# Performance work log

Hardware: AMD Instinct MI355X
Metric: run time of the kernel (lower is better)

Reference implementation:

```python
import jax, jax.numpy as jnp
import numpy as np

N_NODES = 50000


def gcn_conv(x, src, dst, W, b, num_nodes):
    """PyG GCNConv: y = D^{-1/2} (A + I) D^{-1/2} (x @ W) + b.
    src/dst already include self-loops."""
    h = x @ W  # [N, F_out]
    deg = jax.ops.segment_sum(jnp.ones_like(dst, dtype=h.dtype), dst,
                              num_segments=num_nodes)  # in-degree incl. self-loop
    dinv = jnp.where(deg > 0, jax.lax.rsqrt(deg), 0.0)
    norm = dinv[src] * dinv[dst]  # [E]
    msgs = h[src] * norm[:, None]  # gather + scale, [E, F_out]
    out = jax.ops.segment_sum(msgs, dst, num_segments=num_nodes)
    return out + b


def setup_inputs() -> dict:
    key = jax.random.key(0)
    k1, k2, k3, k4 = jax.random.split(key, 4)
    latent, hidden, out_ch = 64, 128, 64
    n_edges = 800000
    z = jax.random.normal(k1, (N_NODES, latent), dtype=jnp.float32)
    edge_index = jax.random.randint(k2, (2, n_edges), 0, N_NODES, dtype=jnp.int64)
    # Glorot-style scaled weights
    W1 = jax.random.normal(k3, (latent, hidden), dtype=jnp.float32) * (1.0 / np.sqrt(latent))
    b1 = jnp.zeros((hidden,), dtype=jnp.float32)
    W2 = jax.random.normal(k4, (hidden, out_ch), dtype=jnp.float32) * (1.0 / np.sqrt(hidden))
    b2 = jnp.zeros((out_ch,), dtype=jnp.float32)
    return {"z": z, "edge_index": edge_index, "W1": W1, "b1": b1, "W2": W2, "b2": b2}


def reference(z, edge_index, W1, b1, W2, b2):
    num_nodes = z.shape[0]
    loops = jnp.arange(num_nodes, dtype=edge_index.dtype)
    src = jnp.concatenate([edge_index[0], loops])  # add self-loops
    dst = jnp.concatenate([edge_index[1], loops])
    x = gcn_conv(z, src, dst, W1, b1, num_nodes)
    x = jax.nn.relu(x)
    x = gcn_conv(x, src, dst, W2, b2, num_nodes)
    x = jax.nn.relu(x)
    return x
```

## Files before the change

### kernel.cpp

```cpp
#include <hip/hip_runtime.h>
#include <hip/hip_fp16.h>

static inline size_t align256(size_t x){ return (x + 255) & ~(size_t)255; }

#define CAP 64
#define NPART 8

__device__ __forceinline__ int detect_is64(const unsigned* __restrict__ e){
  unsigned v = e[2 * (threadIdx.x & 63) + 1];
  return (__ballot(v != 0u) == 0ull) ? 1 : 0;
}

__device__ __forceinline__ int load_idx(const void* edges, long i, int is64){
  return is64 ? (int)((const long long*)edges)[i] : ((const int*)edges)[i];
}

__global__ __launch_bounds__(256) void pack_kernel(const void* __restrict__ edges, int E,
                                                   unsigned* __restrict__ pe,
                                                   int* __restrict__ cnt, int N){
  const int is64 = detect_is64((const unsigned*)edges);
  const int t0 = blockIdx.x * 256 + threadIdx.x;
  const int stride = gridDim.x * 256;
  for (int i = t0; i < N; i += stride) cnt[i] = 0;
  for (int i = t0; i < E; i += stride){
    const unsigned s = (unsigned)load_idx(edges, i, is64);
    const unsigned d = (unsigned)load_idx(edges, (long)E + i, is64);
    pe[i] = (d << 16) | (s & 0xFFFFu);
  }
}

__global__ __launch_bounds__(256) void build_kernel(const unsigned* __restrict__ pe, int E,
                                                    int* __restrict__ cnt,
                                                    unsigned short* __restrict__ csr,
                                                    int N){
  const int p  = blockIdx.x & (NPART - 1);
  const int q  = blockIdx.x >> 3;
  const int nq = gridDim.x >> 3;
  const int nper = (N + NPART - 1) / NPART;
  const int lo = p * nper;
  const int hi = min(lo + nper, N);
  const int stride = nq * 256;
  for (int i = q * 256 + threadIdx.x; i < E; i += stride){
    const unsigned v = pe[i];
    const int d = (int)(v >> 16);
    if (d < lo || d >= hi) continue;
    const int pos = atomicAdd(&cnt[d], 1);
    if (pos < CAP) csr[((size_t)d << 6) + pos] = (unsigned short)(v & 0xFFFFu);
  }
}

__device__ __forceinline__ void h8_acc(uint4 r, float* a){
  const __half2* h = (const __half2*)&r;
  #pragma unroll
  for (int k = 0; k < 4; ++k){
    const float2 f = __half22float2(h[k]);
    a[2*k]     += f.x;
    a[2*k + 1] += f.y;
  }
}

__device__ __forceinline__ void gather8(const uint4* __restrict__ H,
                                        const unsigned short* __restrict__ row,
                                        int deg, int j, float* a){
  int e = 0;
  #pragma unroll 1
  for (; e + 4 <= deg; e += 4){
    const ushort4 rr = *(const ushort4*)(row + e);
    const uint4 v0 = H[(size_t)rr.x * 8 + j];
    const uint4 v1 = H[(size_t)rr.y * 8 + j];
    const uint4 v2 = H[(size_t)rr.z * 8 + j];
    const uint4 v3 = H[(size_t)rr.w * 8 + j];
    h8_acc(v0, a); h8_acc(v1, a); h8_acc(v2, a); h8_acc(v3, a);
  }
  #pragma unroll 1
  for (; e < deg; ++e) h8_acc(H[(size_t)row[e] * 8 + j], a);
}

__global__ __launch_bounds__(256) void prep_kernel(const float4* __restrict__ z,
                                                   uint4* __restrict__ zh,
                                                   const int* __restrict__ cnt,
                                                   float* __restrict__ dinv, int N){
  const int idx = blockIdx.x * 256 + threadIdx.x;
  const int node = idx >> 3;
  if (node >= N) return;
  const int j = idx & 7;
  const float di = rsqrtf((float)(cnt[node] + 1));
  if (j == 0) dinv[node] = di;
  const float4 v0 = z[(size_t)node * 16 + j * 2];
  const float4 v1 = z[(size_t)node * 16 + j * 2 + 1];
  const __half2 a0 = __float22half2_rn(make_float2(di * v0.x, di * v0.y));
  const __half2 a1 = __float22half2_rn(make_float2(di * v0.z, di * v0.w));
  const __half2 a2 = __float22half2_rn(make_float2(di * v1.x, di * v1.y));
  const __half2 a3 = __float22half2_rn(make_float2(di * v1.z, di * v1.w));
  uint4 r;
  r.x = *(const unsigned*)&a0; r.y = *(const unsigned*)&a1;
  r.z = *(const unsigned*)&a2; r.w = *(const unsigned*)&a3;
  zh[idx] = r;
}

__global__ __launch_bounds__(512) void agg_gemm1_kernel(const uint4* __restrict__ zh,
                                                        const unsigned short* __restrict__ csr,
                                                        const int* __restrict__ cnt,
                                                        const float* __restrict__ dinv,
                                                        const float* __restrict__ W1,
                                                        const float* __restrict__ b1,
                                                        float* __restrict__ x1, int N){
  __shared__ float Wl[64 * 128];
  __shared__ float rows[64 * 64];
  const int t = threadIdx.x;

  {
    const float4* Wg = (const float4*)W1;
    float4* Wd = (float4*)Wl;
    #pragma unroll
    for (int i = 0; i < 4; ++i) Wd[t + i * 512] = Wg[t + i * 512];
  }

  const int local = t >> 3;
  const int j = t & 7;
  const int node = blockIdx.x * 64 + local;
  float a[8] = {0.f, 0.f, 0.f, 0.f, 0.f, 0.f, 0.f, 0.f};
  if (node < N){
    h8_acc(zh[(size_t)node * 8 + j], a);
    const int deg = min(cnt[node], CAP);
    gather8(zh, csr + ((size_t)node << 6), deg, j, a);
    const float di = dinv[node];
    #pragma unroll
    for (int k = 0; k < 8; ++k) a[k] *= di;
  }
  float4* rp = (float4*)&rows[t * 8];
  rp[0] = make_float4(a[0], a[1], a[2], a[3]);
  rp[1] = make_float4(a[4], a[5], a[6], a[7]);
  __syncthreads();

  const int jc = t & 127;
  const int g = t >> 7;
  const float bv = b1[jc];
  float accv[16];
  #pragma unroll
  for (int n = 0; n < 16; ++n) accv[n] = bv;

  #pragma unroll 2
  for (int k4 = 0; k4 < 16; ++k4){
    const float w0 = Wl[(4 * k4 + 0) * 128 + jc];
    const float w1 = Wl[(4 * k4 + 1) * 128 + jc];
    const float w2 = Wl[(4 * k4 + 2) * 128 + jc];
    const float w3 = Wl[(4 * k4 + 3) * 128 + jc];
    #pragma unroll
    for (int n = 0; n < 16; ++n){
      const float4 r = ((const float4*)rows)[(g * 16 + n) * 16 + k4];
      accv[n] = fmaf(r.x, w0, accv[n]);
      accv[n] = fmaf(r.y, w1, accv[n]);
      accv[n] = fmaf(r.z, w2, accv[n]);
      accv[n] = fmaf(r.w, w3, accv[n]);
    }
  }

  #pragma unroll
  for (int n = 0; n < 16; ++n){
    const int nn = blockIdx.x * 64 + g * 16 + n;
    if (nn < N) x1[(size_t)nn * 128 + jc] = fmaxf(accv[n], 0.0f);
  }
}

__global__ __launch_bounds__(256) void agg2_kernel(const uint4* __restrict__ X,
                                                   float4* __restrict__ Y,
                                                   const unsigned short* __restrict__ csr,
                                                   const int* __restrict__ cnt,
                                                   const float* __restrict__ dinv,
                                                   const float4* __restrict__ bias,
                                                   int N){
  const int local = threadIdx.x >> 3;
  const int j = threadIdx.x & 7;
  const int node = blockIdx.x * 32 + local;
  if (node >= N) return;
  float a[8] = {0.f, 0.f, 0.f, 0.f, 0.f, 0.f, 0.f, 0.f};
  h8_acc(X[(size_t)node * 8 + j], a);
  const int deg = min(cnt[node], CAP);
  gather8(X, csr + ((size_t)node << 6), deg, j, a);
  const float di = dinv[node];
  const float4 b0 = bias[j * 2];
  const float4 b1v = bias[j * 2 + 1];
  float4 o0, o1;
  o0.x = fmaxf(fmaf(di, a[0], b0.x), 0.f);
  o0.y = fmaxf(fmaf(di, a[1], b0.y), 0.f);
  o0.z = fmaxf(fmaf(di, a[2], b0.z), 0.f);
  o0.w = fmaxf(fmaf(di, a[3], b0.w), 0.f);
  o1.x = fmaxf(fmaf(di, a[4], b1v.x), 0.f);
  o1.y = fmaxf(fmaf(di, a[5], b1v.y), 0.f);
  o1.z = fmaxf(fmaf(di, a[6], b1v.z), 0.f);
  o1.w = fmaxf(fmaf(di, a[7], b1v.w), 0.f);
  Y[(size_t)node * 16 + j * 2] = o0;
  Y[(size_t)node * 16 + j * 2 + 1] = o1;
}

__global__ __launch_bounds__(256) void gemm2_kernel(const float* __restrict__ X,
                                                    const float* __restrict__ W,
                                                    const float* __restrict__ dinv,
                                                    __half* __restrict__ Y, int N){
  constexpr int FIN = 128, FOUT = 64, NT = 32;
  constexpr int G = 256 / FOUT;
  constexpr int NTG = NT / G;
  __shared__ float Wl[FIN * FOUT];
  __shared__ float rows[NT * FIN];
  const int t = threadIdx.x;
  const int node0 = blockIdx.x * NT;

  {
    const float4* Wg = (const float4*)W;
    float4* Wd = (float4*)Wl;
    #pragma unroll
    for (int i = 0; i < FIN * FOUT / 4 / 256; ++i) Wd[t + i * 256] = Wg[t + i * 256];
  }
  {
    float4* rd = (float4*)rows;
    const float4* Xg = (const float4*)X;
    constexpr int TOT = NT * FIN / 4;
    #pragma unroll
    for (int i = 0; i < TOT / 256; ++i){
      const int id = t + i * 256;
      const int n = id / (FIN / 4);
      const int k4 = id % (FIN / 4);
      int node = node0 + n; if (node > N - 1) node = N - 1;
      rd[id] = Xg[(size_t)node * (FIN / 4) + k4];
    }
  }
  __syncthreads();

  const int j = t % FOUT;
  const int g = t / FOUT;
  float acc[NTG];
  #pragma unroll
  for (int n = 0; n < NTG; ++n) acc[n] = 0.0f;

  #pragma unroll 2
  for (int k4 = 0; k4 < FIN / 4; ++k4){
    const float w0 = Wl[(4 * k4 + 0) * FOUT + j];
    const float w1 = Wl[(4 * k4 + 1) * FOUT + j];
    const float w2 = Wl[(4 * k4 + 2) * FOUT + j];
    const float w3 = Wl[(4 * k4 + 3) * FOUT + j];
    #pragma unroll
    for (int n = 0; n < NTG; ++n){
      const float4 r = ((const float4*)rows)[(g * NTG + n) * (FIN / 4) + k4];
      acc[n] = fmaf(r.x, w0, acc[n]);
      acc[n] = fmaf(r.y, w1, acc[n]);
      acc[n] = fmaf(r.z, w2, acc[n]);
      acc[n] = fmaf(r.w, w3, acc[n]);
    }
  }

  #pragma unroll
  for (int n = 0; n < NTG; ++n){
    const int node = node0 + g * NTG + n;
    if (node < N) Y[(size_t)node * FOUT + j] = __float2half(acc[n] * dinv[node]);
  }
}

extern "C" void kernel_launch(void* const* d_in, const int* in_sizes, int n_in,
                              void* d_out, int out_size, void* d_ws, size_t ws_size,
                              hipStream_t stream){
  const float* z  = (const float*)d_in[0];
  const void*  edges = d_in[1];
  const float* W1 = (const float*)d_in[2];
  const float* b1 = (const float*)d_in[3];
  const float* W2 = (const float*)d_in[4];
  const float* b2 = (const float*)d_in[5];
  float* out = (float*)d_out;

  constexpr int F0 = 64, F1 = 128;
  const int N = in_sizes[0] / F0;
  const int E = in_sizes[1] / 2;
  (void)n_in; (void)out_size;

  char* p = (char*)d_ws;
  int*            cnt  = (int*)p;            p += align256((size_t)N * 4);
  float*          dinv = (float*)p;          p += align256((size_t)N * 4);
  unsigned short* csr  = (unsigned short*)p; p += align256((size_t)N * CAP * 2);
  unsigned*       pe   = (unsigned*)p;       p += align256((size_t)E * 4);
  __half*         hbuf = (__half*)p;         p += align256((size_t)N * F0 * 2);
  float*          x1   = (float*)p;          p += align256((size_t)N * F1 * 4);
  (void)ws_size;
  __half* zh = hbuf;
  __half* h2 = hbuf;

  pack_kernel<<<1024, 256, 0, stream>>>(edges, E, pe, cnt, N);
  build_kernel<<<1024, 256, 0, stream>>>(pe, E, cnt, csr, N);
  prep_kernel<<<(N * 8 + 255) / 256, 256, 0, stream>>>(
      (const float4*)z, (uint4*)zh, cnt, dinv, N);

  agg_gemm1_kernel<<<(N + 63) / 64, 512, 0, stream>>>(
      (const uint4*)zh, csr, cnt, dinv, W1, b1, x1, N);

  gemm2_kernel<<<(N + 31) / 32, 256, 0, stream>>>(x1, W2, dinv, h2, N);
  agg2_kernel<<<(N + 31) / 32, 256, 0, stream>>>(
      (const uint4*)h2, (float4*)out, csr, cnt, dinv, (const float4*)b2, N);
}
```

Measured before the change: 199.8 us.

## Fuse second-layer GEMM into first aggregation kernel via shared-memory fp16 tile

Merges gemm2 into the agg+gemm1 kernel. The relu'd hidden activations stay in shared memory as fp16 and are multiplied by W2 right away, so the fp32 x1 buffer of N*128 floats is never written to or read from global memory, and one launch disappears. W1 and W2 are staged in shared memory as fp16 to fit the extra tile, which lowers the precision of the weights and hidden activations. The larger shared-memory footprint and the extra barriers may reduce occupancy of the fused kernel.

```diff
diff --git a/kernel.cpp b/kernel.cpp
--- a/kernel.cpp
+++ b/kernel.cpp
@@ -98,22 +98,31 @@
   zh[idx] = r;
 }
 
-__global__ __launch_bounds__(512) void agg_gemm1_kernel(const uint4* __restrict__ zh,
-                                                        const unsigned short* __restrict__ csr,
-                                                        const int* __restrict__ cnt,
-                                                        const float* __restrict__ dinv,
-                                                        const float* __restrict__ W1,
-                                                        const float* __restrict__ b1,
-                                                        float* __restrict__ x1, int N){
-  __shared__ float Wl[64 * 128];
+#define X1LD 132
+__global__ __launch_bounds__(512) void fused1_kernel(const uint4* __restrict__ zh,
+                                                     const unsigned short* __restrict__ csr,
+                                                     const int* __restrict__ cnt,
+                                                     const float* __restrict__ dinv,
+                                                     const float* __restrict__ W1,
+                                                     const float* __restrict__ b1,
+                                                     const float* __restrict__ W2,
+                                                     __half* __restrict__ h2, int N){
+  __shared__ unsigned short wl[64 * 128];
   __shared__ float rows[64 * 64];
+  __shared__ unsigned short x1t[64 * X1LD];
   const int t = threadIdx.x;
 
   {
     const float4* Wg = (const float4*)W1;
-    float4* Wd = (float4*)Wl;
-    #pragma unroll
-    for (int i = 0; i < 4; ++i) Wd[t + i * 512] = Wg[t + i * 512];
+    #pragma unroll
+    for (int c = 0; c < 4; ++c){
+      const int gi = t + c * 512;
+      const float4 v = Wg[gi];
+      const __half2 h0 = __float22half2_rn(make_float2(v.x, v.y));
+      const __half2 h1 = __float22half2_rn(make_float2(v.z, v.w));
+      uint2 r; r.x = *(const unsigned*)&h0; r.y = *(const unsigned*)&h1;
+      *(uint2*)&wl[gi * 4] = r;
+    }
   }
 
   const int local = t >> 3;
@@ -135,31 +144,97 @@
 
   const int jc = t & 127;
   const int g = t >> 7;
-  const float bv = b1[jc];
-  float accv[16];
-  #pragma unroll
-  for (int n = 0; n < 16; ++n) accv[n] = bv;
-
-  #pragma unroll 2
-  for (int k4 = 0; k4 < 16; ++k4){
-    const float w0 = Wl[(4 * k4 + 0) * 128 + jc];
-    const float w1 = Wl[(4 * k4 + 1) * 128 + jc];
-    const float w2 = Wl[(4 * k4 + 2) * 128 + jc];
-    const float w3 = Wl[(4 * k4 + 3) * 128 + jc];
+  {
+    const float bv = b1[jc];
+    float accv[16];
+    #pragma unroll
+    for (int n = 0; n < 16; ++n) accv[n] = bv;
+
+    #pragma unroll 2
+    for (int k4 = 0; k4 < 16; ++k4){
+      const float w0 = __half2float(*(const __half*)&wl[(4 * k4 + 0) * 128 + jc]);
+      const float w1 = __half2float(*(const __half*)&wl[(4 * k4 + 1) * 128 + jc]);
+      const float w2 = __half2float(*(const __half*)&wl[(4 * k4 + 2) * 128 + jc]);
+      const float w3 = __half2float(*(const __half*)&wl[(4 * k4 + 3) * 128 + jc]);
+      #pragma unroll
+      for (int n = 0; n < 16; ++n){
+        const float4 r = ((const float4*)rows)[(g * 16 + n) * 16 + k4];
+        accv[n] = fmaf(r.x, w0, accv[n]);
+        accv[n] = fmaf(r.y, w1, accv[n]);
+        accv[n] = fmaf(r.z, w2, accv[n]);
+        accv[n] = fmaf(r.w, w3, accv[n]);
+      }
+    }
     #pragma unroll
     for (int n = 0; n < 16; ++n){
-      const float4 r = ((const float4*)rows)[(g * 16 + n) * 16 + k4];
-      accv[n] = fmaf(r.x, w0, accv[n]);
-      accv[n] = fmaf(r.y, w1, accv[n]);
-      accv[n] = fmaf(r.z, w2, accv[n]);
-      accv[n] = fmaf(r.w, w3, accv[n]);
-    }
-  }
-
-  #pragma unroll
-  for (int n = 0; n < 16; ++n){
-    const int nn = blockIdx.x * 64 + g * 16 + n;
-    if (nn < N) x1[(size_t)nn * 128 + jc] = fmaxf(accv[n], 0.0f);
+      const __half hv = __float2half(fmaxf(accv[n], 0.0f));
+      x1t[(g * 16 + n) * X1LD + jc] = *(const unsigned short*)&hv;
+    }
+  }
+  __syncthreads();
+
+  {
+    const float4* Wg = (const float4*)W2;
+    #pragma unroll
+    for (int c = 0; c < 4; ++c){
+      const int gi = t + c * 512;
+      const float4 v = Wg[gi];
+      const __half2 h0 = __float22half2_rn(make_float2(v.x, v.y));
+      const __half2 h1 = __float22half2_rn(make_float2(v.z, v.w));
+      uint2 r; r.x = *(const unsigned*)&h0; r.y = *(const unsigned*)&h1;
+      *(uint2*)&wl[gi * 4] = r;
+    }
+  }
+  __syncthreads();
+
+  const int cg = t & 15;
+  const int ng = t >> 4;
+  const int n0 = ng * 2, n1 = n0 + 1;
+  float acc0[4] = {0.f,0.f,0.f,0.f}, acc1[4] = {0.f,0.f,0.f,0.f};
+  #pragma unroll 4
+  for (int k4 = 0; k4 < 32; ++k4){
+    const int k = k4 * 4;
+    const uint2 xa = *(const uint2*)&x1t[n0 * X1LD + k];
+    const uint2 xb = *(const uint2*)&x1t[n1 * X1LD + k];
+    float xf0[4], xf1[4];
+    {
+      const float2 p0 = __half22float2(*(const __half2*)&xa.x);
+      const float2 p1 = __half22float2(*(const __half2*)&xa.y);
+      xf0[0]=p0.x; xf0[1]=p0.y; xf0[2]=p1.x; xf0[3]=p1.y;
+      const float2 q0 = __half22float2(*(const __half2*)&xb.x);
+      const float2 q1 = __half22float2(*(const __half2*)&xb.y);
+      xf1[0]=q0.x; xf1[1]=q0.y; xf1[2]=q1.x; xf1[3]=q1.y;
+    }
+    #pragma unroll
+    for (int dk = 0; dk < 4; ++dk){
+      const uint2 wv = *(const uint2*)&wl[(k + dk) * 64 + cg * 4];
+      const float2 w01 = __half22float2(*(const __half2*)&wv.x);
+      const float2 w23 = __half22float2(*(const __half2*)&wv.y);
+      acc0[0] = fmaf(xf0[dk], w01.x, acc0[0]);
+      acc0[1] = fmaf(xf0[dk], w01.y, acc0[1]);
+      acc0[2] = fmaf(xf0[dk], w23.x, acc0[2]);
+      acc0[3] = fmaf(xf0[dk], w23.y, acc0[3]);
+      acc1[0] = fmaf(xf1[dk], w01.x, acc1[0]);
+      acc1[1] = fmaf(xf1[dk], w01.y, acc1[1]);
+      acc1[2] = fmaf(xf1[dk], w23.x, acc1[2]);
+      acc1[3] = fmaf(xf1[dk], w23.y, acc1[3]);
+    }
+  }
+  const int gn0 = blockIdx.x * 64 + n0;
+  const int gn1 = gn0 + 1;
+  if (gn0 < N){
+    const float d0 = dinv[gn0];
+    const __half2 h0 = __float22half2_rn(make_float2(acc0[0]*d0, acc0[1]*d0));
+    const __half2 h1 = __float22half2_rn(make_float2(acc0[2]*d0, acc0[3]*d0));
+    uint2 r; r.x = *(const unsigned*)&h0; r.y = *(const unsigned*)&h1;
+    *(uint2*)&h2[(size_t)gn0 * 64 + cg * 4] = r;
+  }
+  if (gn1 < N){
+    const float d1 = dinv[gn1];
+    const __half2 h0 = __float22half2_rn(make_float2(acc1[0]*d1, acc1[1]*d1));
+    const __half2 h1 = __float22half2_rn(make_float2(acc1[2]*d1, acc1[3]*d1));
+    uint2 r; r.x = *(const unsigned*)&h0; r.y = *(const unsigned*)&h1;
+    *(uint2*)&h2[(size_t)gn1 * 64 + cg * 4] = r;
   }
 }
 
@@ -194,68 +269,6 @@
   Y[(size_t)node * 16 + j * 2 + 1] = o1;
 }
 
-__global__ __launch_bounds__(256) void gemm2_kernel(const float* __restrict__ X,
-                                                    const float* __restrict__ W,
-                                                    const float* __restrict__ dinv,
-                                                    __half* __restrict__ Y, int N){
-  constexpr int FIN = 128, FOUT = 64, NT = 32;
-  constexpr int G = 256 / FOUT;
-  constexpr int NTG = NT / G;
-  __shared__ float Wl[FIN * FOUT];
-  __shared__ float rows[NT * FIN];
-  const int t = threadIdx.x;
-  const int node0 = blockIdx.x * NT;
-
-  {
-    const float4* Wg = (const float4*)W;
-    float4* Wd = (float4*)Wl;
-    #pragma unroll
-    for (int i = 0; i < FIN * FOUT / 4 / 256; ++i) Wd[t + i * 256] = Wg[t + i * 256];
-  }
-  {
-    float4* rd = (float4*)rows;
-    const float4* Xg = (const float4*)X;
-    constexpr int TOT = NT * FIN / 4;
-    #pragma unroll
-    for (int i = 0; i < TOT / 256; ++i){
-      const int id = t + i * 256;
-      const int n = id / (FIN / 4);
-      const int k4 = id % (FIN / 4);
-      int node = node0 + n; if (node > N - 1) node = N - 1;
-      rd[id] = Xg[(size_t)node * (FIN / 4) + k4];
-    }
-  }
-  __syncthreads();
-
-  const int j = t % FOUT;
-  const int g = t / FOUT;
-  float acc[NTG];
-  #pragma unroll
-  for (int n = 0; n < NTG; ++n) acc[n] = 0.0f;
-
-  #pragma unroll 2
-  for (int k4 = 0; k4 < FIN / 4; ++k4){
-    const float w0 = Wl[(4 * k4 + 0) * FOUT + j];
-    const float w1 = Wl[(4 * k4 + 1) * FOUT + j];
-    const float w2 = Wl[(4 * k4 + 2) * FOUT + j];
-    const float w3 = Wl[(4 * k4 + 3) * FOUT + j];
-    #pragma unroll
-    for (int n = 0; n < NTG; ++n){
-      const float4 r = ((const float4*)rows)[(g * NTG + n) * (FIN / 4) + k4];
-      acc[n] = fmaf(r.x, w0, acc[n]);
-      acc[n] = fmaf(r.y, w1, acc[n]);
-      acc[n] = fmaf(r.z, w2, acc[n]);
-      acc[n] = fmaf(r.w, w3, acc[n]);
-    }
-  }
-
-  #pragma unroll
-  for (int n = 0; n < NTG; ++n){
-    const int node = node0 + g * NTG + n;
-    if (node < N) Y[(size_t)node * FOUT + j] = __float2half(acc[n] * dinv[node]);
-  }
-}
-
 extern "C" void kernel_launch(void* const* d_in, const int* in_sizes, int n_in,
                               void* d_out, int out_size, void* d_ws, size_t ws_size,
                               hipStream_t stream){
@@ -267,7 +280,7 @@
   const float* b2 = (const float*)d_in[5];
   float* out = (float*)d_out;
 
-  constexpr int F0 = 64, F1 = 128;
+  constexpr int F0 = 64;
   const int N = in_sizes[0] / F0;
   const int E = in_sizes[1] / 2;
   (void)n_in; (void)out_size;
@@ -277,21 +290,18 @@
   float*          dinv = (float*)p;          p += align256((size_t)N * 4);
   unsigned short* csr  = (unsigned short*)p; p += align256((size_t)N * CAP * 2);
   unsigned*       pe   = (unsigned*)p;       p += align256((size_t)E * 4);
-  __half*         hbuf = (__half*)p;         p += align256((size_t)N * F0 * 2);
-  float*          x1   = (float*)p;          p += align256((size_t)N * F1 * 4);
+  __half*         zh   = (__half*)p;         p += align256((size_t)N * F0 * 2);
+  __half*         h2   = (__half*)p;         p += align256((size_t)N * F0 * 2);
   (void)ws_size;
-  __half* zh = hbuf;
-  __half* h2 = hbuf;
 
   pack_kernel<<<1024, 256, 0, stream>>>(edges, E, pe, cnt, N);
   build_kernel<<<1024, 256, 0, stream>>>(pe, E, cnt, csr, N);
   prep_kernel<<<(N * 8 + 255) / 256, 256, 0, stream>>>(
       (const float4*)z, (uint4*)zh, cnt, dinv, N);
 
-  agg_gemm1_kernel<<<(N + 63) / 64, 512, 0, stream>>>(
-      (const uint4*)zh, csr, cnt, dinv, W1, b1, x1, N);
-
-  gemm2_kernel<<<(N + 31) / 32, 256, 0, stream>>>(x1, W2, dinv, h2, N);
+  fused1_kernel<<<(N + 63) / 64, 512, 0, stream>>>(
+      (const uint4*)zh, csr, cnt, dinv, W1, b1, W2, h2, N);
+
   agg2_kernel<<<(N + 31) / 32, 256, 0, stream>>>(
       (const uint4*)h2, (float4*)out, csr, cnt, dinv, (const float4*)b2, N);
 }
```

New measurement: 196.3 us. About the same (-1.8%).
